# Kernel tuning notes

Measured on AMD Instinct MI355X. Metric: run time of the kernel, lower is better.

## Reference

```python
import jax, jax.numpy as jnp
import numpy as np

B, T, C = 4, 4096, 1024
H = 16            # num_heads from init_kwargs
D = C // H        # head_dim = 64
W_SCALE = 0.02    # realistic init scale for weights


def setup_inputs() -> dict:
    key = jax.random.key(0)
    ks = jax.random.split(key, 9)
    inp = {"x": jax.random.normal(ks[0], (B, T, C), dtype=jnp.float32)}
    for i, nm in enumerate(["q", "k", "v", "o"]):
        inp[f"W{nm}"] = jax.random.normal(ks[1 + i], (C, C), dtype=jnp.float32) * W_SCALE
        inp[f"b{nm}"] = jnp.zeros((C,), dtype=jnp.float32)
    return inp


def reference(x, Wq, bq, Wk, bk, Wv, bv, Wo, bo):
    Bx, Tx, Cx = x.shape
    # projections (torch Linear: y = x @ W.T + b), split heads
    q = (x @ Wq.T + bq).reshape(Bx, Tx, H, D)
    k = (x @ Wk.T + bk).reshape(Bx, Tx, H, D)
    v = (x @ Wv.T + bv).reshape(Bx, Tx, H, D)
    # ELU+1 feature map
    q = jax.nn.elu(q) + 1.0
    k = jax.nn.elu(k) + 1.0
    # global KV aggregation: kv[b,h,d,e] = sum_t k[b,t,h,d] * v[b,t,h,e]
    kv = jnp.einsum('bthd,bthe->bhde', k, v)
    # normalizer: q . (sum_t k)
    denom = jnp.einsum('bthd,bhd->bth', q, k.sum(axis=1))
    num = jnp.einsum('bthd,bhde->bthe', q, kv)
    out = num / jnp.clip(denom, 1e-6, None)[..., None]
    out = out.reshape(Bx, Tx, Cx)
    return out @ Wo.T + bo
```

## Files before the change

kernel.cpp:

```cpp
#include <hip/hip_runtime.h>
#include <hip/hip_bf16.h>
#include <stdint.h>


#define B_ 4
#define T_ 4096
#define C_ 1024
#define H_ 16
#define D_ 64
#define M_ (B_*T_)
#define TCH 512
#define K_ 1024
#define NT_ (K_/64)

using u16 = unsigned short;
using u32 = unsigned int;

typedef __attribute__((ext_vector_type(8))) short bf16x8;
typedef __attribute__((ext_vector_type(4))) float f32x4;

static __device__ __forceinline__ u16 f2bf(float f){
  u32 u = __float_as_uint(f);
  u32 r = (u + 0x7fffu + ((u >> 16) & 1u)) >> 16;
  return (u16)r;
}
static __device__ __forceinline__ void unpack8(uint4 u, float* f){
  f[0]=__uint_as_float(u.x<<16); f[1]=__uint_as_float(u.x&0xffff0000u);
  f[2]=__uint_as_float(u.y<<16); f[3]=__uint_as_float(u.y&0xffff0000u);
  f[4]=__uint_as_float(u.z<<16); f[5]=__uint_as_float(u.z&0xffff0000u);
  f[6]=__uint_as_float(u.w<<16); f[7]=__uint_as_float(u.w&0xffff0000u);
}
static __device__ __forceinline__ void gload16(const u16* g, u16* l){
  __builtin_amdgcn_global_load_lds(
      (const __attribute__((address_space(1))) void*)g,
      (__attribute__((address_space(3))) void*)l, 16, 0, 0);
}

#define FENCE() asm volatile("" ::: "memory")
#define BAR() do { FENCE(); __builtin_amdgcn_s_barrier(); FENCE(); } while(0)

__global__ __launch_bounds__(256) void cvt_all(
    const float* __restrict__ x,
    const float* __restrict__ s0, const float* __restrict__ s1,
    const float* __restrict__ s2, const float* __restrict__ s3,
    u16* __restrict__ xb,
    u16* __restrict__ d0, u16* __restrict__ d1,
    u16* __restrict__ d2, u16* __restrict__ d3)
{
  const float* s; u16* d; int bi;
  if (blockIdx.x < 8192) { s = x; d = xb; bi = blockIdx.x; }
  else {
    const int seg = (blockIdx.x - 8192) >> 9;
    bi = (blockIdx.x - 8192) & 511;
    s = seg==0?s0:seg==1?s1:seg==2?s2:s3;
    d = seg==0?d0:seg==1?d1:seg==2?d2:d3;
  }
  const int i = (bi*256 + threadIdx.x) * 8;
  const float4 a = *(const float4*)(s + i);
  const float4 b = *(const float4*)(s + i + 4);
  uint4 o;
  o.x = (u32)f2bf(a.x) | ((u32)f2bf(a.y) << 16);
  o.y = (u32)f2bf(a.z) | ((u32)f2bf(a.w) << 16);
  o.z = (u32)f2bf(b.x) | ((u32)f2bf(b.y) << 16);
  o.w = (u32)f2bf(b.z) | ((u32)f2bf(b.w) << 16);
  *(uint4*)(d + i) = o;
}

template<bool FUSED>
__global__ __launch_bounds__(512, 2) void gemm256(
    const u16* __restrict__ X, const u16* __restrict__ Wm,
    const float* __restrict__ b0, const float* __restrict__ b1,
    const float* __restrict__ b2,
    void* __restrict__ Y0, void* __restrict__ Y1, void* __restrict__ Y2)
{
  extern __shared__ __align__(16) u16 lds[];
  const int tid  = threadIdx.x;
  const int lane = tid & 63, w = tid >> 6;
  const int wr = w >> 2, wc = w & 3;
  const int fr = lane & 15, hi = lane >> 4;

  const int cpx = gridDim.x >> 3;
  const int lin = (blockIdx.x & 7)*cpx + (blockIdx.x >> 3);
  const int bm = lin & 63;
  const int bn = lin >> 6;

  const int srow = tid >> 3;
  const int scc  = (tid & 7) ^ (srow & 7);
  const u16* gA = X  + (size_t)(bm*256 + srow)*K_ + scc*8;
  const u16* gB = Wm + (size_t)(bn*256 + srow)*K_ + scc*8;
  u16* const ldst = lds + tid*8;

  auto stageA = [&](int s, int h, int kt){
    const u16* src = gA + (size_t)(h*128)*K_ + kt*64;
    u16* dst = ldst + s*32768 + h*8192;
    gload16(src, dst);
    gload16(src + (size_t)64*K_, dst + 4096);
  };
  auto stageB = [&](int s, int h, int kt){
    const u16* src = gB + (size_t)(h*128)*K_ + kt*64;
    u16* dst = ldst + s*32768 + 16384 + h*8192;
    gload16(src, dst);
    gload16(src + (size_t)64*K_, dst + 4096);
  };

  f32x4 acc[8][4] = {};
  const int cx0 = (hi ^ (fr & 7)) << 3;
  const int cx1 = ((4 + hi) ^ (fr & 7)) << 3;
  const int br  = (wc & 1) * 64;

  stageB(0,0,0); stageB(0,1,0);
  stageA(0,0,0); stageA(0,1,0);
  stageB(1,0,1); stageB(1,1,1);
  asm volatile("s_waitcnt vmcnt(4)" ::: "memory");
  BAR();

  #pragma unroll 2
  for (int u = 0; u < NT_; ++u) {
    const int s = u & 1;
    const u16* As = lds + s*32768 + wr*8192;
    const u16* Bs = lds + s*32768 + 16384 + (wc>>1)*8192;

    bf16x8 a[4], bv0[4], bv1[4];

    #pragma unroll
    for (int j = 0; j < 4; ++j) bv0[j] = *(const bf16x8*)&Bs[(br + j*16 + fr)*64 + cx0];
    #pragma unroll
    for (int i = 0; i < 4; ++i) a[i]   = *(const bf16x8*)&As[(i*16 + fr)*64 + cx0];
    if (u + 1 < NT_) stageA(s^1, 0, u+1);
    BAR();
    __builtin_amdgcn_s_setprio(1);
    #pragma unroll
    for (int i = 0; i < 4; ++i)
      #pragma unroll
      for (int j = 0; j < 4; ++j)
        acc[i][j] = __builtin_amdgcn_mfma_f32_16x16x32_bf16(a[i], bv0[j], acc[i][j], 0, 0, 0);
    __builtin_amdgcn_s_setprio(0);
    BAR();

    #pragma unroll
    for (int i = 0; i < 4; ++i) a[i] = *(const bf16x8*)&As[((4+i)*16 + fr)*64 + cx0];
    if (u + 1 < NT_) stageA(s^1, 1, u+1);
    BAR();
    __builtin_amdgcn_s_setprio(1);
    #pragma unroll
    for (int i = 0; i < 4; ++i)
      #pragma unroll
      for (int j = 0; j < 4; ++j)
        acc[4+i][j] = __builtin_amdgcn_mfma_f32_16x16x32_bf16(a[i], bv0[j], acc[4+i][j], 0, 0, 0);
    __builtin_amdgcn_s_setprio(0);
    BAR();

    #pragma unroll
    for (int j = 0; j < 4; ++j) bv1[j] = *(const bf16x8*)&Bs[(br + j*16 + fr)*64 + cx1];
    #pragma unroll
    for (int i = 0; i < 4; ++i) a[i]   = *(const bf16x8*)&As[(i*16 + fr)*64 + cx1];
    BAR();
    __builtin_amdgcn_s_setprio(1);
    #pragma unroll
    for (int i = 0; i < 4; ++i)
      #pragma unroll
      for (int j = 0; j < 4; ++j)
        acc[i][j] = __builtin_amdgcn_mfma_f32_16x16x32_bf16(a[i], bv1[j], acc[i][j], 0, 0, 0);
    __builtin_amdgcn_s_setprio(0);
    BAR();

    #pragma unroll
    for (int i = 0; i < 4; ++i) a[i] = *(const bf16x8*)&As[((4+i)*16 + fr)*64 + cx1];
    if (u + 2 < NT_) { stageB(s, 0, u+2); stageB(s, 1, u+2); }
    BAR();
    __builtin_amdgcn_s_setprio(1);
    #pragma unroll
    for (int i = 0; i < 4; ++i)
      #pragma unroll
      for (int j = 0; j < 4; ++j)
        acc[4+i][j] = __builtin_amdgcn_mfma_f32_16x16x32_bf16(a[i], bv1[j], acc[4+i][j], 0, 0, 0);
    __builtin_amdgcn_s_setprio(0);
    if (u + 1 < NT_) {
      if (u + 1 == NT_ - 1) asm volatile("s_waitcnt vmcnt(0)" ::: "memory");
      else                  asm volatile("s_waitcnt vmcnt(4)" ::: "memory");
      BAR();
    }
  }

  const int nloc = wc*64 + fr;
  if constexpr (FUSED) {
    const int sel  = bn >> 2;
    const int colb = (bn & 3)*256 + nloc;
    const float* bp = (sel == 0 ? b0 : sel == 1 ? b1 : b2);
    u16* Y = (u16*)(sel == 0 ? Y0 : sel == 1 ? Y1 : Y2);
    const bool elu = sel < 2;
    float bb[4];
    #pragma unroll
    for (int j = 0; j < 4; ++j) bb[j] = bp[colb + j*16];
    #pragma unroll
    for (int i = 0; i < 8; ++i) {
      #pragma unroll
      for (int r = 0; r < 4; ++r) {
        const size_t row = (size_t)(bm*256 + wr*128 + i*16 + hi*4 + r);
        u16* yp = Y + row*1024 + colb;
        #pragma unroll
        for (int j = 0; j < 4; ++j) {
          float v = acc[i][j][r] + bb[j];
          if (elu) v = (v > 0.0f) ? (v + 1.0f) : __expf(v);
          yp[j*16] = f2bf(v);
        }
      }
    }
  } else {
    const int n0 = bn*256 + nloc;
    float bb[4];
    #pragma unroll
    for (int j = 0; j < 4; ++j) bb[j] = b0[n0 + j*16];
    float* Y = (float*)Y0;
    #pragma unroll
    for (int i = 0; i < 8; ++i) {
      #pragma unroll
      for (int r = 0; r < 4; ++r) {
        const size_t row = (size_t)(bm*256 + wr*128 + i*16 + hi*4 + r);
        float* yp = Y + row*1024 + n0;
        #pragma unroll
        for (int j = 0; j < 4; ++j)
          yp[j*16] = acc[i][j][r] + bb[j];
      }
    }
  }
}

__global__ __launch_bounds__(256) void kv_partial(
    const u16* __restrict__ Kb, const u16* __restrict__ Vb,
    float* __restrict__ kvp, float* __restrict__ ksp)
{
  const int tid = threadIdx.x;
  const int bh = blockIdx.x;
  const int b = bh >> 4, h = bh & 15;
  const int chunk = blockIdx.y;
  __shared__ float kbuf[32][68];
  __shared__ float vbuf[32][68];
  float acc[4][4] = {};
  float ksl = 0.0f;
  const int d0 = (tid >> 4) << 2, e0 = (tid & 15) << 2;
  const int lrow = tid >> 3, lcol = (tid & 7) << 3;

  for (int s = 0; s < TCH/32; ++s) {
    const int t = chunk*TCH + s*32;
    {
      const size_t base = ((size_t)(b*T_ + t + lrow))*C_ + h*64 + lcol;
      const uint4 ku = *(const uint4*)(Kb + base);
      const uint4 vu = *(const uint4*)(Vb + base);
      float kf[8], vf[8];
      unpack8(ku, kf); unpack8(vu, vf);
      #pragma unroll
      for (int j = 0; j < 8; ++j) { kbuf[lrow][lcol+j] = kf[j]; vbuf[lrow][lcol+j] = vf[j]; }
    }
    __syncthreads();
    if (tid < 64) {
      #pragma unroll
      for (int tt = 0; tt < 32; ++tt) ksl += kbuf[tt][tid];
    }
    #pragma unroll
    for (int tt = 0; tt < 32; ++tt) {
      const float4 ka = *(const float4*)&kbuf[tt][d0];
      const float4 va = *(const float4*)&vbuf[tt][e0];
      const float kr[4] = {ka.x, ka.y, ka.z, ka.w};
      const float vr[4] = {va.x, va.y, va.z, va.w};
      #pragma unroll
      for (int i = 0; i < 4; ++i)
        #pragma unroll
        for (int j = 0; j < 4; ++j)
          acc[i][j] = fmaf(kr[i], vr[j], acc[i][j]);
    }
    __syncthreads();
  }

  float* dst = kvp + ((size_t)(chunk*64 + bh))*4096;
  #pragma unroll
  for (int i = 0; i < 4; ++i)
    *(float4*)&dst[(d0+i)*64 + e0] = make_float4(acc[i][0], acc[i][1], acc[i][2], acc[i][3]);
  if (tid < 64) ksp[((size_t)(chunk*64 + bh))*64 + tid] = ksl;
}

__global__ __launch_bounds__(256) void kv_reduce(
    const float* __restrict__ kvp, const float* __restrict__ ksp,
    u16* __restrict__ kvT)
{
  const int idx = blockIdx.x*256 + threadIdx.x;
  if (idx < 262144) {
    float s = 0.0f;
    #pragma unroll
    for (int c = 0; c < 8; ++c) s += kvp[(size_t)c*262144 + idx];
    const int bh = idx >> 12, d = (idx >> 6) & 63, e = idx & 63;
    kvT[(size_t)bh*5120 + e*64 + d] = f2bf(s);
  } else if (idx < 266240) {
    const int i2 = idx - 262144;
    float s = 0.0f;
    #pragma unroll
    for (int c = 0; c < 8; ++c) s += ksp[(size_t)c*4096 + i2];
    const int bh = i2 >> 6, d = i2 & 63;
    kvT[(size_t)bh*5120 + 4096 + d] = f2bf(s);
  } else if (idx < 266240 + 64*15*64) {
    const int i3 = idx - 266240;
    const int bh = i3 / 960, rd = i3 - bh*960;
    kvT[(size_t)bh*5120 + 4160 + rd] = 0;
  }
}

__global__ __launch_bounds__(256) void attn_norm_mfma(
    const u16* __restrict__ Qb, const u16* __restrict__ kvT,
    u16* __restrict__ attn)
{
  __shared__ __align__(16) u16 qs[256*64];
  const int tid = threadIdx.x;
  const int lane = tid & 63, w = tid >> 6;
  const int bh = blockIdx.x;
  const int b = bh >> 4, h = bh & 15;
  const int tt = blockIdx.y;
  const int fr = lane & 15, hi = lane >> 4;

  {
    const int srow = tid >> 3, scc = tid & 7;
    #pragma unroll
    for (int r = 0; r < 8; ++r) {
      const int row = r*32 + srow;
      const u16* src = Qb + ((size_t)(b*T_ + tt*256 + row))*C_ + h*64
                         + ((scc ^ (row & 7)) << 3);
      gload16(src, qs + tid*8 + r*2048);
    }
  }

  const u16* kvb = kvT + (size_t)bh*5120;
  bf16x8 bv[5][2];
  #pragma unroll
  for (int j = 0; j < 5; ++j) {
    const int row = (j < 4) ? (j*16 + fr) : (64 + fr);
    bv[j][0] = *(const bf16x8*)&kvb[row*64 + hi*8];
    bv[j][1] = *(const bf16x8*)&kvb[row*64 + 32 + hi*8];
  }

  __syncthreads();

  f32x4 accN[4][4] = {};
  f32x4 accD[4] = {};
  #pragma unroll
  for (int kh = 0; kh < 2; ++kh) {
    const int cx = ((kh*4 + hi) ^ (fr & 7)) << 3;
    bf16x8 a[4];
    #pragma unroll
    for (int i = 0; i < 4; ++i)
      a[i] = *(const bf16x8*)&qs[(w*64 + i*16 + fr)*64 + cx];
    #pragma unroll
    for (int i = 0; i < 4; ++i) {
      #pragma unroll
      for (int j = 0; j < 4; ++j)
        accN[i][j] = __builtin_amdgcn_mfma_f32_16x16x32_bf16(a[i], bv[j][kh], accN[i][j], 0, 0, 0);
      accD[i] = __builtin_amdgcn_mfma_f32_16x16x32_bf16(a[i], bv[4][kh], accD[i], 0, 0, 0);
    }
  }

  #pragma unroll
  for (int i = 0; i < 4; ++i) {
    #pragma unroll
    for (int r = 0; r < 4; ++r) {
      const float den = __shfl(accD[i][r], lane & 0x30);
      const float inv = 1.0f / fmaxf(den, 1e-6f);
      const size_t row = (size_t)(b*T_ + tt*256 + w*64 + i*16 + hi*4 + r);
      u16* yp = attn + row*1024 + h*64 + fr;
      #pragma unroll
      for (int j = 0; j < 4; ++j)
        yp[j*16] = f2bf(accN[i][j][r] * inv);
    }
  }
}

extern "C" void kernel_launch(void* const* d_in, const int* in_sizes, int n_in,
                              void* d_out, int out_size, void* d_ws, size_t ws_size,
                              hipStream_t stream)
{
  (void)in_sizes; (void)n_in; (void)out_size; (void)ws_size;
  const float* x  = (const float*)d_in[0];
  const float* Wq = (const float*)d_in[1];
  const float* bq = (const float*)d_in[2];
  const float* Wk = (const float*)d_in[3];
  const float* bk = (const float*)d_in[4];
  const float* Wv = (const float*)d_in[5];
  const float* bv = (const float*)d_in[6];
  const float* Wo = (const float*)d_in[7];
  const float* bo = (const float*)d_in[8];
  float* out = (float*)d_out;
  char* ws = (char*)d_ws;

  const size_t MB = 1024*1024;
  u16*   xb   = (u16*)(ws);
  u16*   wqb  = (u16*)(ws + 32*MB);
  u16*   wkb  = (u16*)(ws + 34*MB);
  u16*   wvb  = (u16*)(ws + 36*MB);
  u16*   wob  = (u16*)(ws + 38*MB);
  u16*   q    = (u16*)(ws + 40*MB);
  u16*   k    = (u16*)(ws + 72*MB);
  u16*   v    = (u16*)(ws + 104*MB);
  float* kvp  = (float*)(ws + 136*MB);
  float* ksp  = (float*)(ws + 144*MB);
  u16*   kvT  = (u16*)(ws + 144*MB + 131072);
  u16*   attn = xb;

  static bool s_attr_done = false;
  if (!s_attr_done) {
    (void)hipFuncSetAttribute(reinterpret_cast<const void*>(gemm256<true>),
                              hipFuncAttributeMaxDynamicSharedMemorySize, 131072);
    (void)hipFuncSetAttribute(reinterpret_cast<const void*>(gemm256<false>),
                              hipFuncAttributeMaxDynamicSharedMemorySize, 131072);
    s_attr_done = true;
  }

  dim3 blk(256);
  cvt_all<<<dim3(8192 + 4*512), blk, 0, stream>>>(
      x, Wq, Wk, Wv, Wo, xb, wqb, wkb, wvb, wob);

  gemm256<true><<<dim3(64*12), dim3(512), 131072, stream>>>(
      xb, wqb, bq, bk, bv, q, k, v);

  kv_partial<<<dim3(B_*H_, T_/TCH), blk, 0, stream>>>(k, v, kvp, ksp);
  kv_reduce<<<dim3(1280), blk, 0, stream>>>(kvp, ksp, kvT);
  attn_norm_mfma<<<dim3(B_*H_, T_/256), blk, 0, stream>>>(q, kvT, attn);

  gemm256<false><<<dim3(64*4), dim3(512), 131072, stream>>>(
      attn, wob, bo, bo, bo, out, out, out);
}
```

Before: 226.8 us.

## Triple-buffer A tiles with prefetch distance two and patch-based block swizzle

The GEMM now keeps A in a three-slot LDS ring and B in two slots, prefetching both two k-steps ahead. It also spreads the B loads across two phases of the loop body. Block indices are remapped into 4x4 patches per XCD to improve L2 reuse of A and B tiles. LDS rises from 128 KiB to 160 KiB per block. That likely drops occupancy from two blocks per CU to one, trading latency hiding across blocks for deeper in-block prefetch.

```diff
diff --git a/kernel.cpp b/kernel.cpp
--- a/kernel.cpp
+++ b/kernel.cpp
@@ -79,26 +79,30 @@
   const int wr = w >> 2, wc = w & 3;
   const int fr = lane & 15, hi = lane >> 4;
 
-  const int cpx = gridDim.x >> 3;
-  const int lin = (blockIdx.x & 7)*cpx + (blockIdx.x >> 3);
-  const int bm = lin & 63;
-  const int bn = lin >> 6;
+  const int xcd = blockIdx.x & 7;
+  const int r   = blockIdx.x >> 3;
+  const int ppx = gridDim.x >> 7;
+  const int patchIdx = xcd * ppx + (r >> 4);
+  const int wi = r & 15;
+  const int pm = FUSED ? (patchIdx & 15) : patchIdx;
+  const int pn = FUSED ? (patchIdx >> 4) : 0;
+  const int bm = pm*4 + (wi & 3);
+  const int bn = pn*4 + (wi >> 2);
 
   const int srow = tid >> 3;
   const int scc  = (tid & 7) ^ (srow & 7);
   const u16* gA = X  + (size_t)(bm*256 + srow)*K_ + scc*8;
   const u16* gB = Wm + (size_t)(bn*256 + srow)*K_ + scc*8;
-  u16* const ldst = lds + tid*8;
-
-  auto stageA = [&](int s, int h, int kt){
+
+  auto stageA = [&](int slot, int h, int kt){
     const u16* src = gA + (size_t)(h*128)*K_ + kt*64;
-    u16* dst = ldst + s*32768 + h*8192;
+    u16* dst = lds + slot*16384 + h*8192 + tid*8;
     gload16(src, dst);
     gload16(src + (size_t)64*K_, dst + 4096);
   };
-  auto stageB = [&](int s, int h, int kt){
+  auto stageB = [&](int slot, int h, int kt){
     const u16* src = gB + (size_t)(h*128)*K_ + kt*64;
-    u16* dst = ldst + s*32768 + 16384 + h*8192;
+    u16* dst = lds + 49152 + slot*16384 + h*8192 + tid*8;
     gload16(src, dst);
     gload16(src + (size_t)64*K_, dst + 4096);
   };
@@ -108,17 +112,21 @@
   const int cx1 = ((4 + hi) ^ (fr & 7)) << 3;
   const int br  = (wc & 1) * 64;
 
+  stageA(0,0,0); stageA(0,1,0);
   stageB(0,0,0); stageB(0,1,0);
-  stageA(0,0,0); stageA(0,1,0);
+  stageA(1,0,1); stageA(1,1,1);
   stageB(1,0,1); stageB(1,1,1);
-  asm volatile("s_waitcnt vmcnt(4)" ::: "memory");
+  asm volatile("s_waitcnt vmcnt(8)" ::: "memory");
   BAR();
 
+  int aslot = 0;
   #pragma unroll 2
-  for (int u = 0; u < NT_; ++u) {
-    const int s = u & 1;
-    const u16* As = lds + s*32768 + wr*8192;
-    const u16* Bs = lds + s*32768 + 16384 + (wc>>1)*8192;
+  for (int v = 0; v < NT_; ++v) {
+    const int bslot  = v & 1;
+    const int astage = (aslot == 0) ? 2 : aslot - 1;
+    const bool more  = (v + 2 < NT_);
+    const u16* As = lds + aslot*16384 + wr*8192;
+    const u16* Bs = lds + 49152 + bslot*16384 + (wc>>1)*8192;
 
     bf16x8 a[4], bv0[4], bv1[4];
 
@@ -126,7 +134,7 @@
     for (int j = 0; j < 4; ++j) bv0[j] = *(const bf16x8*)&Bs[(br + j*16 + fr)*64 + cx0];
     #pragma unroll
     for (int i = 0; i < 4; ++i) a[i]   = *(const bf16x8*)&As[(i*16 + fr)*64 + cx0];
-    if (u + 1 < NT_) stageA(s^1, 0, u+1);
+    if (more) stageA(astage, 0, v+2);
     BAR();
     __builtin_amdgcn_s_setprio(1);
     #pragma unroll
@@ -139,7 +147,7 @@
 
     #pragma unroll
     for (int i = 0; i < 4; ++i) a[i] = *(const bf16x8*)&As[((4+i)*16 + fr)*64 + cx0];
-    if (u + 1 < NT_) stageA(s^1, 1, u+1);
+    if (more) stageA(astage, 1, v+2);
     BAR();
     __builtin_amdgcn_s_setprio(1);
     #pragma unroll
@@ -154,6 +162,7 @@
     for (int j = 0; j < 4; ++j) bv1[j] = *(const bf16x8*)&Bs[(br + j*16 + fr)*64 + cx1];
     #pragma unroll
     for (int i = 0; i < 4; ++i) a[i]   = *(const bf16x8*)&As[(i*16 + fr)*64 + cx1];
+    if (more) stageB(bslot, 0, v+2);
     BAR();
     __builtin_amdgcn_s_setprio(1);
     #pragma unroll
@@ -166,7 +175,7 @@
 
     #pragma unroll
     for (int i = 0; i < 4; ++i) a[i] = *(const bf16x8*)&As[((4+i)*16 + fr)*64 + cx1];
-    if (u + 2 < NT_) { stageB(s, 0, u+2); stageB(s, 1, u+2); }
+    if (more) stageB(bslot, 1, v+2);
     BAR();
     __builtin_amdgcn_s_setprio(1);
     #pragma unroll
@@ -175,11 +184,12 @@
       for (int j = 0; j < 4; ++j)
         acc[4+i][j] = __builtin_amdgcn_mfma_f32_16x16x32_bf16(a[i], bv1[j], acc[4+i][j], 0, 0, 0);
     __builtin_amdgcn_s_setprio(0);
-    if (u + 1 < NT_) {
-      if (u + 1 == NT_ - 1) asm volatile("s_waitcnt vmcnt(0)" ::: "memory");
-      else                  asm volatile("s_waitcnt vmcnt(4)" ::: "memory");
+    if (v + 1 < NT_) {
+      if (more) asm volatile("s_waitcnt vmcnt(8)" ::: "memory");
+      else      asm volatile("s_waitcnt vmcnt(0)" ::: "memory");
       BAR();
     }
+    aslot = (aslot == 2) ? 0 : aslot + 1;
   }
 
   const int nloc = wc*64 + fr;
@@ -195,14 +205,14 @@
     #pragma unroll
     for (int i = 0; i < 8; ++i) {
       #pragma unroll
-      for (int r = 0; r < 4; ++r) {
-        const size_t row = (size_t)(bm*256 + wr*128 + i*16 + hi*4 + r);
+      for (int r2 = 0; r2 < 4; ++r2) {
+        const size_t row = (size_t)(bm*256 + wr*128 + i*16 + hi*4 + r2);
         u16* yp = Y + row*1024 + colb;
         #pragma unroll
         for (int j = 0; j < 4; ++j) {
-          float v = acc[i][j][r] + bb[j];
-          if (elu) v = (v > 0.0f) ? (v + 1.0f) : __expf(v);
-          yp[j*16] = f2bf(v);
+          float vv = acc[i][j][r2] + bb[j];
+          if (elu) vv = (vv > 0.0f) ? (vv + 1.0f) : __expf(vv);
+          yp[j*16] = f2bf(vv);
         }
       }
     }
@@ -215,12 +225,12 @@
     #pragma unroll
     for (int i = 0; i < 8; ++i) {
       #pragma unroll
-      for (int r = 0; r < 4; ++r) {
-        const size_t row = (size_t)(bm*256 + wr*128 + i*16 + hi*4 + r);
+      for (int r2 = 0; r2 < 4; ++r2) {
+        const size_t row = (size_t)(bm*256 + wr*128 + i*16 + hi*4 + r2);
         float* yp = Y + row*1024 + n0;
         #pragma unroll
         for (int j = 0; j < 4; ++j)
-          yp[j*16] = acc[i][j][r] + bb[j];
+          yp[j*16] = acc[i][j][r2] + bb[j];
       }
     }
   }
@@ -405,9 +415,9 @@
   static bool s_attr_done = false;
   if (!s_attr_done) {
     (void)hipFuncSetAttribute(reinterpret_cast<const void*>(gemm256<true>),
-                              hipFuncAttributeMaxDynamicSharedMemorySize, 131072);
+                              hipFuncAttributeMaxDynamicSharedMemorySize, 163840);
     (void)hipFuncSetAttribute(reinterpret_cast<const void*>(gemm256<false>),
-                              hipFuncAttributeMaxDynamicSharedMemorySize, 131072);
+                              hipFuncAttributeMaxDynamicSharedMemorySize, 163840);
     s_attr_done = true;
   }
 
@@ -415,13 +425,13 @@
   cvt_all<<<dim3(8192 + 4*512), blk, 0, stream>>>(
       x, Wq, Wk, Wv, Wo, xb, wqb, wkb, wvb, wob);
 
-  gemm256<true><<<dim3(64*12), dim3(512), 131072, stream>>>(
+  gemm256<true><<<dim3(64*12), dim3(512), 163840, stream>>>(
       xb, wqb, bq, bk, bv, q, k, v);
 
   kv_partial<<<dim3(B_*H_, T_/TCH), blk, 0, stream>>>(k, v, kvp, ksp);
   kv_reduce<<<dim3(1280), blk, 0, stream>>>(kvp, ksp, kvT);
   attn_norm_mfma<<<dim3(B_*H_, T_/256), blk, 0, stream>>>(q, kvT, attn);
 
-  gemm256<false><<<dim3(64*4), dim3(512), 131072, stream>>>(
+  gemm256<false><<<dim3(64*4), dim3(512), 163840, stream>>>(
       attn, wob, bo, bo, bo, out, out, out);
 }
```

Result: faster. 220.9 us (-2.6%).
